# Kernel optimization log

Measured on AMD Instinct MI355X. Metric: run time of the kernel, lower is better.

## Reference

```python
import jax, jax.numpy as jnp
import numpy as np

NUM_SAMPLE = 10   # self._num, hard-coded as range(10) in prob_sample
FSCALE = 5        # neighbor-count kernel
CSCALE = 3        # constraint-count kernel
EPS = 1e-16


def _sum_window(x, k):
    # x: [N,H,W] -> SAME-padded k x k box sum == F.conv2d with ones(1,1,k,k), padding=(k-1)//2
    return jax.lax.reduce_window(x, 0.0, jax.lax.add, (1, k, k), (1, 1, 1), 'SAME')


def _dilate8(x):
    # 3x3 max-pool = one step of 8-connectivity dilation (skimage flood_fill default
    # connectivity for 2D is full connectivity when my_connectivity is None)
    return jax.lax.reduce_window(x, 0.0, jax.lax.max, (1, 3, 3), (1, 1, 1), 'SAME')


def _flood_fill(fg, seed_r, seed_c):
    # fg: [N,H,W] binary float; returns the fg-connected component containing the seed,
    # via fixed-point iteration of masked dilation (equivalent to skimage.flood_fill
    # seeded at the max-neighbor pixel, then thresholding the filled value).
    N, H, W = fg.shape
    reach0 = jnp.zeros_like(fg).at[jnp.arange(N), seed_r, seed_c].set(1.0) * fg

    def cond(st):
        _, changed, it = st
        return changed & (it < H * W)

    def body(st):
        reach, _, it = st
        new = jnp.maximum(reach, _dilate8(reach) * fg)
        return new, jnp.any(new > reach), it + 1

    reach, _, _ = jax.lax.while_loop(cond, body, (reach0, jnp.array(True), jnp.int32(0)))
    return reach


def connectivity_rewards(sample_ns, fg_num):
    # sample_ns: [n, S, H, W] int class indices. Returns binary rewards [n, S, H, W]
    # (reward_type='binary', run_state='train'). All (image, sample) pairs processed
    # in one batched flood fill per foreground class.
    n, S, H, W = sample_ns.shape
    flat = sample_ns.reshape(n * S, H, W)
    total = jnp.zeros((n * S, H, W), jnp.float32)
    for class_idx in range(1, fg_num):  # small fixed loop over fg classes
        fg = (flat == class_idx).astype(jnp.float32)
        neigh = _sum_window(fg, FSCALE) * fg           # count_neighbor * fg
        neigh_flat = neigh.reshape(n * S, H * W)
        seed = jnp.argmax(neigh_flat, axis=-1)          # pixel with max neighbor count
        has_fg = (jnp.max(neigh_flat, axis=-1) > 0).astype(jnp.float32)
        fill = _flood_fill(fg, seed // W, seed % W) * has_fg[:, None, None]
        Fc = _sum_window(fill, CSCALE) * fill           # F_fg_neigbors
        Sc = _sum_window(fg, CSCALE) * fg               # S_fg_neigbors
        r = (jnp.where(Fc == 0, -1.0, Fc) == jnp.where(Sc == 0, -2.0, Sc)).astype(jnp.float32)
        total = total + r
    return total.reshape(n, S, H, W)


def setup_inputs() -> dict:
    key = jax.random.key(0)
    logits = jax.random.normal(key, (4, 4, 512, 512), dtype=jnp.float32)
    preds = jax.nn.softmax(logits, axis=1)  # per-pixel class probabilities [n,c,h,w]
    return {"preds": preds}


def reference(preds):
    n, c, h, w = preds.shape
    skey = jax.random.key(42)
    # prob_sample: per-pixel multinomial over classes, repeated NUM_SAMPLE times
    lg = jnp.moveaxis(jnp.log(preds + EPS), 1, -1)  # [n,h,w,c]
    samp = jax.random.categorical(skey, lg, axis=-1, shape=(NUM_SAMPLE, n, h, w))
    sample_ns = jnp.transpose(samp, (1, 0, 2, 3)).astype(jnp.int32)  # [n,S,h,w]
    prob_ns = jnp.take_along_axis(preds, sample_ns, axis=1)          # [n,S,h,w]
    rewards = jax.lax.stop_gradient(connectivity_rewards(sample_ns, c))
    # REINFORCE objective: maximize reward-weighted log-prob of sampled labelings
    loss = -(rewards * jnp.log(prob_ns + EPS)).mean()
    return loss
```

## Files before the change

kernel.cpp:

```cpp
#include <hip/hip_runtime.h>
#include <stdint.h>

#define JAX_PARTITIONABLE 1

#define SNUM 10
#define NBATCH 4
#define NCLS 4
#define HH 512
#define WW 512
#define IMG (HH*WW)
#define NPIX (SNUM*NBATCH*IMG)
#define GUMTOT ((uint32_t)NPIX*NCLS)
#define HALFG (GUMTOT/2u)
#define WPI (IMG/32)
#define QCAP 3584

#if __has_builtin(__builtin_amdgcn_alignbit)
__device__ __forceinline__ uint32_t rotl32(uint32_t x, int r) {
  return __builtin_amdgcn_alignbit(x, x, (uint32_t)(32 - r));
}
#else
__device__ __forceinline__ uint32_t rotl32(uint32_t x, int r) {
  return (x << r) | (x >> (32 - r));
}
#endif

__device__ __forceinline__ void tf2x32(uint32_t x0, uint32_t x1,
                                       uint32_t& o0, uint32_t& o1) {
  const uint32_t k0 = 0u, k1 = 42u;
  const uint32_t k2 = k0 ^ k1 ^ 0x1BD11BDAu;
  x0 += k0; x1 += k1;
#define TFR(r) { x0 += x1; x1 = rotl32(x1, (r)); x1 ^= x0; }
  TFR(13) TFR(15) TFR(26) TFR(6)
  x0 += k1; x1 += k2 + 1u;
  TFR(17) TFR(29) TFR(16) TFR(24)
  x0 += k2; x1 += k0 + 2u;
  TFR(13) TFR(15) TFR(26) TFR(6)
  x0 += k0; x1 += k1 + 3u;
  TFR(17) TFR(29) TFR(16) TFR(24)
  x0 += k1; x1 += k2 + 4u;
  TFR(13) TFR(15) TFR(26) TFR(6)
  x0 += k2; x1 += k0 + 5u;
#undef TFR
  o0 = x0; o1 = x1;
}

__device__ __forceinline__ float u01(uint32_t bits) {
  float f = __uint_as_float((bits >> 9) | 0x3f800000u) - 1.0f;
  const float tiny = 1.17549435e-38f;
  f = f + tiny;
  return fmaxf(tiny, f);
}

__device__ __forceinline__ uint32_t gum_bits(uint32_t g) {
#if JAX_PARTITIONABLE
  uint32_t y0, y1;
  tf2x32(0u, g, y0, y1);
  return y0 ^ y1;
#else
  uint32_t y0, y1;
  uint32_t j = (g < HALFG) ? g : (g - HALFG);
  tf2x32(j, j + HALFG, y0, y1);
  return (g < HALFG) ? y0 : y1;
#endif
}

__device__ __forceinline__ uint32_t unpack32(uint64_t v) {
  uint64_t tt = v | (v >> 1);
  uint64_t u = ~tt & 0x5555555555555555ULL;
  u = (u ^ (u >> 1))  & 0x3333333333333333ULL;
  u = (u ^ (u >> 2))  & 0x0F0F0F0F0F0F0F0FULL;
  u = (u ^ (u >> 4))  & 0x00FF00FF00FF00FFULL;
  u = (u ^ (u >> 8))  & 0x0000FFFF0000FFFFULL;
  u = (u ^ (u >> 16)) & 0x00000000FFFFFFFFULL;
  return (uint32_t)u;
}

__global__ __launch_bounds__(256) void k_sample(const float* __restrict__ preds,
                                                uint8_t* __restrict__ packed,
                                                float* __restrict__ acc,
                                                uint32_t* __restrict__ gkey) {
  const int t = blockIdx.x * 256 + threadIdx.x;
  if (t == 0) acc[0] = 0.0f;
  if (t < 120) gkey[t] = 0u;
  const int sn = t >> 16;
  const int n  = sn & 3;
  const int pg = t & 65535;
  const int pix = pg << 2;

  float pp[NCLS][4];
#pragma unroll
  for (int c = 0; c < NCLS; ++c) {
    const float4 v = *reinterpret_cast<const float4*>(
        preds + (((int64_t)(n * NCLS + c)) << 18) + pix);
    pp[c][0] = v.x + 1e-16f;
    pp[c][1] = v.y + 1e-16f;
    pp[c][2] = v.z + 1e-16f;
    pp[c][3] = v.w + 1e-16f;
  }

  const uint32_t gb = (uint32_t)sn * 1048576u + ((uint32_t)pix << 2);
  uint32_t byte = 0;
#pragma unroll
  for (int j = 0; j < 4; ++j) {
    float bp = pp[0][j];
    float be = -__log2f(u01(gum_bits(gb + (uint32_t)(j * 4))));
    int bc = 0;
#pragma unroll
    for (int c = 1; c < NCLS; ++c) {
      float ec = -__log2f(u01(gum_bits(gb + (uint32_t)(j * 4 + c))));
      if (pp[c][j] * be > bp * ec) { bp = pp[c][j]; be = ec; bc = c; }
    }
    byte |= (uint32_t)bc << (2 * j);
  }
  packed[t] = (uint8_t)byte;
}

__global__ __launch_bounds__(256) void k_argmax(const uint8_t* __restrict__ packed,
                                                uint32_t* __restrict__ gkey) {
  __shared__ uint32_t sfg[36 * 16];
  __shared__ uint32_t skey;
  const int tid = threadIdx.x;
  const int b = blockIdx.x;
  const int prob = b >> 4;
  const int slab = b & 15;
  const int sn = prob % 40;
  const int k  = 1 + prob / 40;
  if (tid == 0) skey = 0u;

  const uint64_t* p64 = reinterpret_cast<const uint64_t*>(packed);
  const uint64_t pat = (uint64_t)k * 0x5555555555555555ULL;
  const int gr0 = slab * 32 - 2;
  for (int wi = tid; wi < 36 * 16; wi += 256) {
    const int gr = gr0 + (wi >> 4);
    uint32_t m = 0;
    if (gr >= 0 && gr < HH)
      m = unpack32(p64[(int64_t)sn * WPI + (gr << 4) + (wi & 15)] ^ pat);
    sfg[wi] = m;
  }
  __syncthreads();

  uint32_t lbest = 0;
  for (int idx = tid; idx < 512; idx += 256) {
    const int rl = 2 + (idx >> 4);
    const int col = idx & 15;
    const uint32_t cw = sfg[(rl << 4) + col];
    if (!cw) continue;
    uint64_t rb[5];
#pragma unroll
    for (int d = 0; d < 5; ++d) {
      const int base = ((rl + d - 2) << 4) + col;
      const uint32_t le = (col > 0)  ? sfg[base - 1] : 0u;
      const uint32_t cu = sfg[base];
      const uint32_t ri = (col < 15) ? sfg[base + 1] : 0u;
      rb[d] = ((uint64_t)(ri & 7u) << 34) | ((uint64_t)cu << 2) | (uint64_t)(le >> 30);
    }
    const int gr = slab * 32 + (idx >> 4);
    uint32_t bits = cw;
    while (bits) {
      const int j = __ffs(bits) - 1;
      bits &= bits - 1;
      int cnt = 0;
#pragma unroll
      for (int d = 0; d < 5; ++d)
        cnt += __popc((uint32_t)(rb[d] >> j) & 0x1fu);
      const uint32_t fidx = (uint32_t)((gr << 9) + (col << 5) + j);
      const uint32_t key = ((uint32_t)cnt << 18) | (0x3FFFFu - fidx);
      lbest = lbest > key ? lbest : key;
    }
  }
#pragma unroll
  for (int off = 32; off > 0; off >>= 1) {
    const uint32_t o = (uint32_t)__shfl_down((int)lbest, off, 64);
    lbest = lbest > o ? lbest : o;
  }
  if ((threadIdx.x & 63) == 0 && lbest) atomicMax(&skey, lbest);
  __syncthreads();
  if (tid == 0 && skey) atomicMax(&gkey[prob], skey);
}


__device__ __forceinline__ uint32_t runmask(uint32_t m, uint32_t s) {
  uint32_t out = 0;
  while (s) {
    const int j = __ffs(s) - 1;
    const uint32_t bj = 1u << j;
    const uint32_t up = ((m + bj) ^ m) & m;
    const uint32_t rm = __brev(m);
    const uint32_t rbj = 1u << (31 - j);
    const uint32_t dn = __brev(((rm + rbj) ^ rm) & rm);
    const uint32_t run = up | dn;
    out |= run;
    s &= ~run;
  }
  return out;
}

__device__ __forceinline__ void claimf(uint32_t* fg, uint32_t* qw, uint32_t* qb,
                                       uint32_t* qtail, uint32_t t, uint32_t want) {
  const uint32_t old = atomicAnd(&fg[t], ~want);
  uint32_t nb = old & want;
  if (!nb) return;
  const uint32_t ext = runmask(old, nb) & ~nb;
  if (ext) {
    const uint32_t old2 = atomicAnd(&fg[t], ~ext);
    nb |= old2 & ext;
  }
  const uint32_t slot = atomicAdd(qtail, 1u);
  if (slot < QCAP) { qw[slot] = t; qb[slot] = nb; }
}

__device__ __forceinline__ uint64_t shup64(uint64_t v) {
  const uint32_t lo = __shfl_up((unsigned int)v, 1, 64);
  const uint32_t hi = __shfl_up((unsigned int)(v >> 32), 1, 64);
  return ((uint64_t)hi << 32) | lo;
}
__device__ __forceinline__ uint64_t shdn64(uint64_t v) {
  const uint32_t lo = __shfl_down((unsigned int)v, 1, 64);
  const uint32_t hi = __shfl_down((unsigned int)(v >> 32), 1, 64);
  return ((uint64_t)hi << 32) | lo;
}

__global__ __launch_bounds__(64) void k_fill(const float* __restrict__ preds,
                                             const uint8_t* __restrict__ packed,
                                             const uint32_t* __restrict__ gkey,
                                             float* __restrict__ acc) {
  __shared__ uint32_t fg[WPI];
  __shared__ uint32_t qw[QCAP];
  __shared__ uint32_t qb[QCAP];
  __shared__ uint32_t qtail;
  const int tid = threadIdx.x;
  const int prob = blockIdx.x;
  const int sn = prob % 40;
  const int k  = 1 + prob / 40;
  const int n  = sn & 3;

  const uint32_t bkey = gkey[prob];
  if ((bkey >> 18) == 0u) return;

  const uint32_t seed = 0x3FFFFu - (bkey & 0x3FFFFu);
  const int sr = (int)(seed >> 9), sc = (int)(seed & 511);
  const float* chan = preds + (((int64_t)n) * NCLS + k) * (int64_t)IMG;
  const uint64_t* p64 = reinterpret_cast<const uint64_t*>(packed);
  const uint64_t pat = (uint64_t)k * 0x5555555555555555ULL;
  float local = 0.0f;

  int r0 = sr - 31; if (r0 < 0) r0 = 0; if (r0 > HH - 64) r0 = HH - 64;
  int cl = (sc >> 5) - (((sc & 31) < 16) ? 1 : 0);
  if (cl < 0) cl = 0; if (cl > 14) cl = 14;
  const int ar = r0 + tid;
  const int64_t pb = (int64_t)sn * WPI + (ar << 4) + cl;
  const uint64_t fgw = ((uint64_t)unpack32(p64[pb + 1] ^ pat) << 32)
                     |            unpack32(p64[pb]     ^ pat);
  uint64_t fill = (ar == sr) ? (1ULL << (sc - (cl << 5))) : 0ULL;

  bool conv = false;
  for (int it = 0; it < 2048; ++it) {
    uint64_t up = shup64(fill); if (tid == 0)  up = 0ULL;
    uint64_t dn = shdn64(fill); if (tid == 63) dn = 0ULL;
    const uint64_t sp = fill | up | dn;
    const uint64_t nf = (fgw & (sp | (sp << 1) | (sp >> 1))) | fill;
    const bool ch = (nf != fill);
    fill = nf;
    if (__ballot(ch) == 0ULL) { conv = true; break; }
  }

  bool esc = !conv;
  if (fill) {
    if (tid == 0 && r0 > 0) esc = true;
    if (tid == 63 && r0 + 63 < HH - 1) esc = true;
    if ((fill & 1ULL) && cl > 0) esc = true;
    if ((fill >> 63) && cl < 14) esc = true;
  }

  if (__ballot(esc) == 0ULL) {
    uint64_t bits = fill;
    const float* rowp = chan + (int64_t)ar * WW + (cl << 5);
    while (bits) {
      const int j = __ffsll((unsigned long long)bits) - 1;
      bits &= bits - 1;
      local += logf(rowp[j] + 1e-16f);
    }
  } else {
    if (tid == 0) qtail = 0u;
    for (int wi = tid; wi < WPI; wi += 64)
      fg[wi] = unpack32(p64[(int64_t)sn * WPI + wi] ^ pat);
    __syncthreads();
    claimf(fg, qw, qb, &qtail, seed >> 5, 1u << (seed & 31));
    uint32_t head = 0;
    while (true) {
      uint32_t tail = atomicAdd(&qtail, 0u);
      if (tail > QCAP) tail = QCAP;
      if (head >= tail) break;
      for (uint32_t i = head + (uint32_t)tid; i < tail; i += 64) {
        const uint32_t w = qw[i], got = qb[i];
        const int row = (int)(w >> 4), cb = (int)(w & 15);
        const uint32_t spread = got | (got << 1) | (got >> 1);
        const bool lo = (got & 1u) != 0u, hi = (got >> 31) != 0u;
        if (row > 0) {
          claimf(fg, qw, qb, &qtail, w - 16, spread);
          if (cb > 0 && lo)  claimf(fg, qw, qb, &qtail, w - 17, 0x80000000u);
          if (cb < 15 && hi) claimf(fg, qw, qb, &qtail, w - 15, 1u);
        }
        if (row < HH - 1) {
          claimf(fg, qw, qb, &qtail, w + 16, spread);
          if (cb > 0 && lo)  claimf(fg, qw, qb, &qtail, w + 15, 0x80000000u);
          if (cb < 15 && hi) claimf(fg, qw, qb, &qtail, w + 17, 1u);
        }
        if (cb > 0 && lo)  claimf(fg, qw, qb, &qtail, w - 1, 0x80000000u);
        if (cb < 15 && hi) claimf(fg, qw, qb, &qtail, w + 1, 1u);
      }
      head = tail;
    }
    uint32_t tot = qtail; if (tot > QCAP) tot = QCAP;
    for (uint32_t i = (uint32_t)tid; i < tot; i += 64) {
      const uint32_t w = qw[i];
      uint32_t bits = qb[i];
      const int row = (int)(w >> 4);
      const int colb = (int)(w & 15) << 5;
      const float* rowp = chan + (int64_t)row * WW;
      while (bits) {
        const int j = __ffs(bits) - 1;
        bits &= bits - 1;
        local += logf(rowp[colb + j] + 1e-16f);
      }
    }
  }

#pragma unroll
  for (int off = 32; off > 0; off >>= 1)
    local += __shfl_down(local, off, 64);
  if (tid == 0 && local != 0.0f)
    atomicAdd(acc, local);
}

__global__ void k_final(const float* __restrict__ acc, float* __restrict__ out) {
  out[0] = -acc[0] / 10485760.0f;
}

extern "C" void kernel_launch(void* const* d_in, const int* in_sizes, int n_in,
                              void* d_out, int out_size, void* d_ws, size_t ws_size,
                              hipStream_t stream) {
  const float* preds = (const float*)d_in[0];
  float* out = (float*)d_out;
  float* acc = (float*)d_ws;
  uint32_t* gkey = (uint32_t*)((char*)d_ws + 64);
  uint8_t* packed = (uint8_t*)d_ws + 4096;

  k_sample<<<10240, 256, 0, stream>>>(preds, packed, acc, gkey);
  k_argmax<<<1920, 256, 0, stream>>>(packed, gkey);
  k_fill<<<120, 64, 0, stream>>>(preds, packed, gkey, acc);
  k_final<<<1, 1, 0, stream>>>(acc, out);
}
```

Before: 162.0 us.

## Fuse argmax, flood-fill and final reduction into one kernel with flag sync

```diff
diff --git a/kernel.cpp b/kernel.cpp
--- a/kernel.cpp
+++ b/kernel.cpp
@@ -14,6 +14,7 @@
 #define HALFG (GUMTOT/2u)
 #define WPI (IMG/32)
 #define QCAP 3584
+#define NARG 1920
 
 #if __has_builtin(__builtin_amdgcn_alignbit)
 __device__ __forceinline__ uint32_t rotl32(uint32_t x, int r) {
@@ -46,10 +47,8 @@
 }
 
 __device__ __forceinline__ float u01(uint32_t bits) {
-  float f = __uint_as_float((bits >> 9) | 0x3f800000u) - 1.0f;
-  const float tiny = 1.17549435e-38f;
-  f = f + tiny;
-  return fmaxf(tiny, f);
+  const float f = __uint_as_float((bits >> 9) | 0x3f800000u) - 1.0f;
+  return fmaxf(f, 1.17549435e-38f);
 }
 
 __device__ __forceinline__ uint32_t gum_bits(uint32_t g) {
@@ -79,10 +78,13 @@
 __global__ __launch_bounds__(256) void k_sample(const float* __restrict__ preds,
                                                 uint8_t* __restrict__ packed,
                                                 float* __restrict__ acc,
-                                                uint32_t* __restrict__ gkey) {
+                                                uint32_t* __restrict__ gkey,
+                                                uint32_t* __restrict__ argdone,
+                                                uint32_t* __restrict__ misc) {
   const int t = blockIdx.x * 256 + threadIdx.x;
   if (t == 0) acc[0] = 0.0f;
-  if (t < 120) gkey[t] = 0u;
+  if (t < 120) { gkey[t] = 0u; argdone[t] = 0u; }
+  if (t == 120) { misc[0] = 0u; misc[1] = 0u; misc[2] = 0u; }
   const int sn = t >> 16;
   const int n  = sn & 3;
   const int pg = t & 65535;
@@ -93,10 +95,7 @@
   for (int c = 0; c < NCLS; ++c) {
     const float4 v = *reinterpret_cast<const float4*>(
         preds + (((int64_t)(n * NCLS + c)) << 18) + pix);
-    pp[c][0] = v.x + 1e-16f;
-    pp[c][1] = v.y + 1e-16f;
-    pp[c][2] = v.z + 1e-16f;
-    pp[c][3] = v.w + 1e-16f;
+    pp[c][0] = v.x; pp[c][1] = v.y; pp[c][2] = v.z; pp[c][3] = v.w;
   }
 
   const uint32_t gb = (uint32_t)sn * 1048576u + ((uint32_t)pix << 2);
@@ -104,79 +103,16 @@
 #pragma unroll
   for (int j = 0; j < 4; ++j) {
     float bp = pp[0][j];
-    float be = -__log2f(u01(gum_bits(gb + (uint32_t)(j * 4))));
+    float bl = __log2f(u01(gum_bits(gb + (uint32_t)(j * 4))));
     int bc = 0;
 #pragma unroll
     for (int c = 1; c < NCLS; ++c) {
-      float ec = -__log2f(u01(gum_bits(gb + (uint32_t)(j * 4 + c))));
-      if (pp[c][j] * be > bp * ec) { bp = pp[c][j]; be = ec; bc = c; }
+      const float lc = __log2f(u01(gum_bits(gb + (uint32_t)(j * 4 + c))));
+      if (pp[c][j] * bl < bp * lc) { bp = pp[c][j]; bl = lc; bc = c; }
     }
     byte |= (uint32_t)bc << (2 * j);
   }
   packed[t] = (uint8_t)byte;
-}
-
-__global__ __launch_bounds__(256) void k_argmax(const uint8_t* __restrict__ packed,
-                                                uint32_t* __restrict__ gkey) {
-  __shared__ uint32_t sfg[36 * 16];
-  __shared__ uint32_t skey;
-  const int tid = threadIdx.x;
-  const int b = blockIdx.x;
-  const int prob = b >> 4;
-  const int slab = b & 15;
-  const int sn = prob % 40;
-  const int k  = 1 + prob / 40;
-  if (tid == 0) skey = 0u;
-
-  const uint64_t* p64 = reinterpret_cast<const uint64_t*>(packed);
-  const uint64_t pat = (uint64_t)k * 0x5555555555555555ULL;
-  const int gr0 = slab * 32 - 2;
-  for (int wi = tid; wi < 36 * 16; wi += 256) {
-    const int gr = gr0 + (wi >> 4);
-    uint32_t m = 0;
-    if (gr >= 0 && gr < HH)
-      m = unpack32(p64[(int64_t)sn * WPI + (gr << 4) + (wi & 15)] ^ pat);
-    sfg[wi] = m;
-  }
-  __syncthreads();
-
-  uint32_t lbest = 0;
-  for (int idx = tid; idx < 512; idx += 256) {
-    const int rl = 2 + (idx >> 4);
-    const int col = idx & 15;
-    const uint32_t cw = sfg[(rl << 4) + col];
-    if (!cw) continue;
-    uint64_t rb[5];
-#pragma unroll
-    for (int d = 0; d < 5; ++d) {
-      const int base = ((rl + d - 2) << 4) + col;
-      const uint32_t le = (col > 0)  ? sfg[base - 1] : 0u;
-      const uint32_t cu = sfg[base];
-      const uint32_t ri = (col < 15) ? sfg[base + 1] : 0u;
-      rb[d] = ((uint64_t)(ri & 7u) << 34) | ((uint64_t)cu << 2) | (uint64_t)(le >> 30);
-    }
-    const int gr = slab * 32 + (idx >> 4);
-    uint32_t bits = cw;
-    while (bits) {
-      const int j = __ffs(bits) - 1;
-      bits &= bits - 1;
-      int cnt = 0;
-#pragma unroll
-      for (int d = 0; d < 5; ++d)
-        cnt += __popc((uint32_t)(rb[d] >> j) & 0x1fu);
-      const uint32_t fidx = (uint32_t)((gr << 9) + (col << 5) + j);
-      const uint32_t key = ((uint32_t)cnt << 18) | (0x3FFFFu - fidx);
-      lbest = lbest > key ? lbest : key;
-    }
-  }
-#pragma unroll
-  for (int off = 32; off > 0; off >>= 1) {
-    const uint32_t o = (uint32_t)__shfl_down((int)lbest, off, 64);
-    lbest = lbest > o ? lbest : o;
-  }
-  if ((threadIdx.x & 63) == 0 && lbest) atomicMax(&skey, lbest);
-  __syncthreads();
-  if (tid == 0 && skey) atomicMax(&gkey[prob], skey);
 }
 
 
@@ -221,108 +157,192 @@
   return ((uint64_t)hi << 32) | lo;
 }
 
-__global__ __launch_bounds__(64) void k_fill(const float* __restrict__ preds,
-                                             const uint8_t* __restrict__ packed,
-                                             const uint32_t* __restrict__ gkey,
-                                             float* __restrict__ acc) {
-  __shared__ uint32_t fg[WPI];
-  __shared__ uint32_t qw[QCAP];
-  __shared__ uint32_t qb[QCAP];
-  __shared__ uint32_t qtail;
+__global__ __launch_bounds__(256) void k_fused(const float* __restrict__ preds,
+                                               const uint8_t* __restrict__ packed,
+                                               uint32_t* __restrict__ gkey,
+                                               uint32_t* __restrict__ argdone,
+                                               uint32_t* __restrict__ misc,
+                                               uint32_t* __restrict__ fgg,
+                                               uint32_t* __restrict__ qwg,
+                                               uint32_t* __restrict__ qbg,
+                                               float* __restrict__ acc,
+                                               float* __restrict__ out) {
   const int tid = threadIdx.x;
-  const int prob = blockIdx.x;
+  const int b = blockIdx.x;
+  const uint64_t* p64 = reinterpret_cast<const uint64_t*>(packed);
+
+  if (b < NARG) {
+    __shared__ uint32_t sfg[36 * 16];
+    __shared__ uint32_t skey;
+    const int prob = b >> 4;
+    const int slab = b & 15;
+    const int sn = prob % 40;
+    const int k  = 1 + prob / 40;
+    if (tid == 0) skey = 0u;
+
+    const uint64_t pat = (uint64_t)k * 0x5555555555555555ULL;
+    const int gr0 = slab * 32 - 2;
+    for (int wi = tid; wi < 36 * 16; wi += 256) {
+      const int gr = gr0 + (wi >> 4);
+      uint32_t m = 0;
+      if (gr >= 0 && gr < HH)
+        m = unpack32(p64[(int64_t)sn * WPI + (gr << 4) + (wi & 15)] ^ pat);
+      sfg[wi] = m;
+    }
+    __syncthreads();
+
+    uint32_t lbest = 0;
+    for (int idx = tid; idx < 512; idx += 256) {
+      const int rl = 2 + (idx >> 4);
+      const int col = idx & 15;
+      const uint32_t cw = sfg[(rl << 4) + col];
+      if (!cw) continue;
+      uint64_t rb[5];
+#pragma unroll
+      for (int d = 0; d < 5; ++d) {
+        const int base = ((rl + d - 2) << 4) + col;
+        const uint32_t le = (col > 0)  ? sfg[base - 1] : 0u;
+        const uint32_t cu = sfg[base];
+        const uint32_t ri = (col < 15) ? sfg[base + 1] : 0u;
+        rb[d] = ((uint64_t)(ri & 7u) << 34) | ((uint64_t)cu << 2) | (uint64_t)(le >> 30);
+      }
+      const int gr = slab * 32 + (idx >> 4);
+      uint32_t bits = cw;
+      while (bits) {
+        const int j = __ffs(bits) - 1;
+        bits &= bits - 1;
+        int cnt = 0;
+#pragma unroll
+        for (int d = 0; d < 5; ++d)
+          cnt += __popc((uint32_t)(rb[d] >> j) & 0x1fu);
+        const uint32_t fidx = (uint32_t)((gr << 9) + (col << 5) + j);
+        const uint32_t key = ((uint32_t)cnt << 18) | (0x3FFFFu - fidx);
+        lbest = lbest > key ? lbest : key;
+      }
+    }
+#pragma unroll
+    for (int off = 32; off > 0; off >>= 1) {
+      const uint32_t o = (uint32_t)__shfl_down((int)lbest, off, 64);
+      lbest = lbest > o ? lbest : o;
+    }
+    if ((tid & 63) == 0 && lbest) atomicMax(&skey, lbest);
+    __syncthreads();
+    if (tid == 0) {
+      if (skey) atomicMax(&gkey[prob], skey);
+      __threadfence();
+      atomicAdd(&argdone[prob], 1u);
+    }
+    return;
+  }
+
+  const int prob = b - NARG;
+  if (tid == 0) {
+    while (atomicAdd(&argdone[prob], 0u) < 16u) __builtin_amdgcn_s_sleep(2);
+  }
+  __syncthreads();
+  if (tid >= 64) return;
+
   const int sn = prob % 40;
   const int k  = 1 + prob / 40;
   const int n  = sn & 3;
-
-  const uint32_t bkey = gkey[prob];
-  if ((bkey >> 18) == 0u) return;
-
-  const uint32_t seed = 0x3FFFFu - (bkey & 0x3FFFFu);
-  const int sr = (int)(seed >> 9), sc = (int)(seed & 511);
+  const uint64_t pat = (uint64_t)k * 0x5555555555555555ULL;
   const float* chan = preds + (((int64_t)n) * NCLS + k) * (int64_t)IMG;
-  const uint64_t* p64 = reinterpret_cast<const uint64_t*>(packed);
-  const uint64_t pat = (uint64_t)k * 0x5555555555555555ULL;
+  uint32_t* filldone = misc + 0;
+  uint32_t* lock     = misc + 1;
+  uint32_t* qtail    = misc + 2;
+
   float local = 0.0f;
-
-  int r0 = sr - 31; if (r0 < 0) r0 = 0; if (r0 > HH - 64) r0 = HH - 64;
-  int cl = (sc >> 5) - (((sc & 31) < 16) ? 1 : 0);
-  if (cl < 0) cl = 0; if (cl > 14) cl = 14;
-  const int ar = r0 + tid;
-  const int64_t pb = (int64_t)sn * WPI + (ar << 4) + cl;
-  const uint64_t fgw = ((uint64_t)unpack32(p64[pb + 1] ^ pat) << 32)
-                     |            unpack32(p64[pb]     ^ pat);
-  uint64_t fill = (ar == sr) ? (1ULL << (sc - (cl << 5))) : 0ULL;
-
-  bool conv = false;
-  for (int it = 0; it < 2048; ++it) {
-    uint64_t up = shup64(fill); if (tid == 0)  up = 0ULL;
-    uint64_t dn = shdn64(fill); if (tid == 63) dn = 0ULL;
-    const uint64_t sp = fill | up | dn;
-    const uint64_t nf = (fgw & (sp | (sp << 1) | (sp >> 1))) | fill;
-    const bool ch = (nf != fill);
-    fill = nf;
-    if (__ballot(ch) == 0ULL) { conv = true; break; }
-  }
-
-  bool esc = !conv;
-  if (fill) {
-    if (tid == 0 && r0 > 0) esc = true;
-    if (tid == 63 && r0 + 63 < HH - 1) esc = true;
-    if ((fill & 1ULL) && cl > 0) esc = true;
-    if ((fill >> 63) && cl < 14) esc = true;
-  }
-
-  if (__ballot(esc) == 0ULL) {
-    uint64_t bits = fill;
-    const float* rowp = chan + (int64_t)ar * WW + (cl << 5);
-    while (bits) {
-      const int j = __ffsll((unsigned long long)bits) - 1;
-      bits &= bits - 1;
-      local += logf(rowp[j] + 1e-16f);
-    }
-  } else {
-    if (tid == 0) qtail = 0u;
-    for (int wi = tid; wi < WPI; wi += 64)
-      fg[wi] = unpack32(p64[(int64_t)sn * WPI + wi] ^ pat);
-    __syncthreads();
-    claimf(fg, qw, qb, &qtail, seed >> 5, 1u << (seed & 31));
-    uint32_t head = 0;
-    while (true) {
-      uint32_t tail = atomicAdd(&qtail, 0u);
-      if (tail > QCAP) tail = QCAP;
-      if (head >= tail) break;
-      for (uint32_t i = head + (uint32_t)tid; i < tail; i += 64) {
-        const uint32_t w = qw[i], got = qb[i];
-        const int row = (int)(w >> 4), cb = (int)(w & 15);
-        const uint32_t spread = got | (got << 1) | (got >> 1);
-        const bool lo = (got & 1u) != 0u, hi = (got >> 31) != 0u;
-        if (row > 0) {
-          claimf(fg, qw, qb, &qtail, w - 16, spread);
-          if (cb > 0 && lo)  claimf(fg, qw, qb, &qtail, w - 17, 0x80000000u);
-          if (cb < 15 && hi) claimf(fg, qw, qb, &qtail, w - 15, 1u);
+  const uint32_t bkey = atomicMax(&gkey[prob], 0u);
+  if ((bkey >> 18) != 0u) {
+    const uint32_t seed = 0x3FFFFu - (bkey & 0x3FFFFu);
+    const int sr = (int)(seed >> 9), sc = (int)(seed & 511);
+
+    int r0 = sr - 31; if (r0 < 0) r0 = 0; if (r0 > HH - 64) r0 = HH - 64;
+    int cl = (sc >> 5) - (((sc & 31) < 16) ? 1 : 0);
+    if (cl < 0) cl = 0; if (cl > 14) cl = 14;
+    const int ar = r0 + tid;
+    const int64_t pb = (int64_t)sn * WPI + (ar << 4) + cl;
+    const uint64_t fgw = ((uint64_t)unpack32(p64[pb + 1] ^ pat) << 32)
+                       |            unpack32(p64[pb]     ^ pat);
+    uint64_t fill = (ar == sr) ? (1ULL << (sc - (cl << 5))) : 0ULL;
+
+    bool conv = false;
+    for (int it = 0; it < 2048; ++it) {
+      uint64_t up = shup64(fill); if (tid == 0)  up = 0ULL;
+      uint64_t dn = shdn64(fill); if (tid == 63) dn = 0ULL;
+      const uint64_t sp = fill | up | dn;
+      const uint64_t nf = (fgw & (sp | (sp << 1) | (sp >> 1))) | fill;
+      const bool ch = (nf != fill);
+      fill = nf;
+      if (__ballot(ch) == 0ULL) { conv = true; break; }
+    }
+
+    bool esc = !conv;
+    if (fill) {
+      if (tid == 0 && r0 > 0) esc = true;
+      if (tid == 63 && r0 + 63 < HH - 1) esc = true;
+      if ((fill & 1ULL) && cl > 0) esc = true;
+      if ((fill >> 63) && cl < 14) esc = true;
+    }
+
+    if (__ballot(esc) == 0ULL) {
+      uint64_t bits = fill;
+      const float* rowp = chan + (int64_t)ar * WW + (cl << 5);
+      while (bits) {
+        const int j = __ffsll((unsigned long long)bits) - 1;
+        bits &= bits - 1;
+        local += logf(rowp[j] + 1e-16f);
+      }
+    } else {
+      if (tid == 0) {
+        while (atomicCAS(lock, 0u, 1u) != 0u) __builtin_amdgcn_s_sleep(8);
+      }
+      for (int wi = tid; wi < WPI; wi += 64)
+        atomicExch(&fgg[wi], unpack32(p64[(int64_t)sn * WPI + wi] ^ pat));
+      claimf(fgg, qwg, qbg, qtail, seed >> 5, 1u << (seed & 31));
+      uint32_t head = 0;
+      while (true) {
+        uint32_t tail = atomicAdd(qtail, 0u);
+        if (tail > QCAP) tail = QCAP;
+        if (head >= tail) break;
+        for (uint32_t i = head + (uint32_t)tid; i < tail; i += 64) {
+          const uint32_t w = qwg[i], got = qbg[i];
+          const int row = (int)(w >> 4), cb = (int)(w & 15);
+          const uint32_t spread = got | (got << 1) | (got >> 1);
+          const bool lo = (got & 1u) != 0u, hi = (got >> 31) != 0u;
+          if (row > 0) {
+            claimf(fgg, qwg, qbg, qtail, w - 16, spread);
+            if (cb > 0 && lo)  claimf(fgg, qwg, qbg, qtail, w - 17, 0x80000000u);
+            if (cb < 15 && hi) claimf(fgg, qwg, qbg, qtail, w - 15, 1u);
+          }
+          if (row < HH - 1) {
+            claimf(fgg, qwg, qbg, qtail, w + 16, spread);
+            if (cb > 0 && lo)  claimf(fgg, qwg, qbg, qtail, w + 15, 0x80000000u);
+            if (cb < 15 && hi) claimf(fgg, qwg, qbg, qtail, w + 17, 1u);
+          }
+          if (cb > 0 && lo)  claimf(fgg, qwg, qbg, qtail, w - 1, 0x80000000u);
+          if (cb < 15 && hi) claimf(fgg, qwg, qbg, qtail, w + 1, 1u);
         }
-        if (row < HH - 1) {
-          claimf(fg, qw, qb, &qtail, w + 16, spread);
-          if (cb > 0 && lo)  claimf(fg, qw, qb, &qtail, w + 15, 0x80000000u);
-          if (cb < 15 && hi) claimf(fg, qw, qb, &qtail, w + 17, 1u);
+        head = tail;
+      }
+      uint32_t tot = atomicAdd(qtail, 0u); if (tot > QCAP) tot = QCAP;
+      for (uint32_t i = (uint32_t)tid; i < tot; i += 64) {
+        const uint32_t w = qwg[i];
+        uint32_t bits = qbg[i];
+        const int row = (int)(w >> 4);
+        const int colb = (int)(w & 15) << 5;
+        const float* rowp = chan + (int64_t)row * WW;
+        while (bits) {
+          const int j = __ffs(bits) - 1;
+          bits &= bits - 1;
+          local += logf(rowp[colb + j] + 1e-16f);
         }
-        if (cb > 0 && lo)  claimf(fg, qw, qb, &qtail, w - 1, 0x80000000u);
-        if (cb < 15 && hi) claimf(fg, qw, qb, &qtail, w + 1, 1u);
-      }
-      head = tail;
-    }
-    uint32_t tot = qtail; if (tot > QCAP) tot = QCAP;
-    for (uint32_t i = (uint32_t)tid; i < tot; i += 64) {
-      const uint32_t w = qw[i];
-      uint32_t bits = qb[i];
-      const int row = (int)(w >> 4);
-      const int colb = (int)(w & 15) << 5;
-      const float* rowp = chan + (int64_t)row * WW;
-      while (bits) {
-        const int j = __ffs(bits) - 1;
-        bits &= bits - 1;
-        local += logf(rowp[colb + j] + 1e-16f);
+      }
+      if (tid == 0) {
+        __threadfence();
+        atomicExch(qtail, 0u);
+        __threadfence();
+        atomicExch(lock, 0u);
       }
     }
   }
@@ -330,12 +350,15 @@
 #pragma unroll
   for (int off = 32; off > 0; off >>= 1)
     local += __shfl_down(local, off, 64);
-  if (tid == 0 && local != 0.0f)
-    atomicAdd(acc, local);
-}
-
-__global__ void k_final(const float* __restrict__ acc, float* __restrict__ out) {
-  out[0] = -acc[0] / 10485760.0f;
+  if (tid == 0) {
+    if (local != 0.0f) atomicAdd(acc, local);
+    __threadfence();
+    const uint32_t old = atomicAdd(filldone, 1u);
+    if (old == 119u) {
+      const float s = atomicAdd(acc, 0.0f);
+      out[0] = -s / 10485760.0f;
+    }
+  }
 }
 
 extern "C" void kernel_launch(void* const* d_in, const int* in_sizes, int n_in,
@@ -343,12 +366,17 @@
                               hipStream_t stream) {
   const float* preds = (const float*)d_in[0];
   float* out = (float*)d_out;
-  float* acc = (float*)d_ws;
-  uint32_t* gkey = (uint32_t*)((char*)d_ws + 64);
-  uint8_t* packed = (uint8_t*)d_ws + 4096;
-
-  k_sample<<<10240, 256, 0, stream>>>(preds, packed, acc, gkey);
-  k_argmax<<<1920, 256, 0, stream>>>(packed, gkey);
-  k_fill<<<120, 64, 0, stream>>>(preds, packed, gkey, acc);
-  k_final<<<1, 1, 0, stream>>>(acc, out);
-}
+  char* ws = (char*)d_ws;
+  float*    acc     = (float*)ws;
+  uint32_t* gkey    = (uint32_t*)(ws + 64);
+  uint32_t* argdone = (uint32_t*)(ws + 1024);
+  uint32_t* misc    = (uint32_t*)(ws + 1536);
+  uint8_t*  packed  = (uint8_t*)(ws + 4096);
+  uint32_t* fgg     = (uint32_t*)(ws + (3u << 20));
+  uint32_t* qwg     = (uint32_t*)(ws + (3u << 20) + (64u << 10));
+  uint32_t* qbg     = (uint32_t*)(ws + (3u << 20) + (96u << 10));
+
+  k_sample<<<10240, 256, 0, stream>>>(preds, packed, acc, gkey, argdone, misc);
+  k_fused<<<NARG + 120, 256, 0, stream>>>(preds, packed, gkey, argdone, misc,
+                                          fgg, qwg, qbg, acc, out);
+}
```

Result: slower. 185.0 us (+14.2%).
